# Kernel optimization log

Measured on AMD Instinct MI355X. Metric: run time of the kernel, lower is better.

## Reference

```python
import jax, jax.numpy as jnp
import numpy as np

EMBED_DIM = 200
INPUT_DIM = 512


def setup_inputs() -> dict:
    key = jax.random.key(0)
    k1, k2, k3, k4 = jax.random.split(key, 4)
    B, L, T = 64, 256, 64
    x = jax.random.normal(k1, (B, L, INPUT_DIM), dtype=jnp.float32)
    y = jax.random.normal(k2, (B, T, INPUT_DIM), dtype=jnp.float32)
    # fc = nn.Linear(input_dim, embedding_dim)
    W = jax.random.normal(k3, (EMBED_DIM, INPUT_DIM), dtype=jnp.float32) * (1.0 / np.sqrt(INPUT_DIM))
    b = jax.random.normal(k4, (EMBED_DIM,), dtype=jnp.float32) * 0.01
    return {"x": x, "y": y, "W": W, "b": b}


def reference(x, y, W, b):
    # Project both modalities (last dim != embedding_dim in original triggers fc)
    xp = jnp.einsum('bld,ed->ble', x, W) + b   # B x L x E
    yp = jnp.einsum('btd,ed->bte', y, W) + b   # B x T x E
    # Pairwise matchmap: for pair (i, j), matchmap = xp[i] @ yp[j].T -> L x T
    mm = jnp.einsum('ile,jte->ijlt', xp, yp)   # B x B x L x T
    # MISA: max over L (rows of matchmap, dim 0), then mean over T
    S = jnp.max(mm, axis=2).mean(axis=2)       # B x B
    return S
```

## Files before the change

### kernel.cpp

```cpp
#include <hip/hip_runtime.h>
#include <hip/hip_bf16.h>
#include <stdint.h>

#define BB 64
#define LL 256
#define TT 64
#define DD 512
#define EE 200
#define EP 208
#define NKK 13
#define NROWS_X 16384
#define BSTRIDE 264

typedef __attribute__((ext_vector_type(8))) short short8;
typedef __attribute__((ext_vector_type(4))) float floatx4;
typedef __attribute__((ext_vector_type(16))) float floatx16;

__device__ __forceinline__ short f2bf(float f) {
  uint32_t u = __builtin_bit_cast(uint32_t, f);
  u = (u + 0x7fffu + ((u >> 16) & 1u)) >> 16;
  return (short)u;
}

__device__ __forceinline__ uint32_t pack2(float lo, float hi) {
  return __builtin_amdgcn_perm(__builtin_bit_cast(uint32_t, hi),
                               __builtin_bit_cast(uint32_t, lo), 0x07060302u);
}

typedef const __attribute__((address_space(1))) uint32_t gu32_t;
typedef __attribute__((address_space(3))) uint32_t lu32_t;
__device__ __forceinline__ void glds16(const void* g, void* l) {
  __builtin_amdgcn_global_load_lds((gu32_t*)g, (lu32_t*)l, 16, 0, 0);
}

#define VMCNT_BARRIER(N) asm volatile("s_waitcnt vmcnt(" #N ")\n\ts_barrier" ::: "memory")

__global__ void wcvt_kernel(const float* __restrict__ W, short* __restrict__ Wb) {
  const int t = blockIdx.x * 256 + threadIdx.x;
  const int base = t * 8;
  const int e = base >> 9;
  short8 o;
  if (e < EE) {
    const floatx4 f0 = *(const floatx4*)(W + base);
    const floatx4 f1 = *(const floatx4*)(W + base + 4);
    o[0] = f2bf(f0.x); o[1] = f2bf(f0.y); o[2] = f2bf(f0.z); o[3] = f2bf(f0.w);
    o[4] = f2bf(f1.x); o[5] = f2bf(f1.y); o[6] = f2bf(f1.z); o[7] = f2bf(f1.w);
  } else {
    o = (short8)0;
  }
  *(short8*)(Wb + base) = o;
}

__global__ __launch_bounds__(256, 2) void proj_kernel(const float* __restrict__ x,
                                                      const float* __restrict__ y,
                                                      const short* __restrict__ Wb,
                                                      const float* __restrict__ bias,
                                                      short* __restrict__ pT) {
  __shared__ __align__(16) char smem[73728];
  float* ldsA = (float*)smem;
  short* ldsB = (short*)(smem + 24576);
  short* bounce = (short*)smem;

  const int tid  = threadIdx.x;
  const int lane = tid & 63;
  const int wid  = tid >> 6;
  const int r16   = lane & 15;
  const int khalf = lane >> 4;

  const int row0 = blockIdx.x * 64;
  const float* srcbase = (row0 < NROWS_X) ? (x + (size_t)row0 * DD)
                                          : (y + (size_t)(row0 - NROWS_X) * DD);

  floatx4 acc[NKK];
#pragma unroll
  for (int n = 0; n < NKK; n++) acc[n] = (floatx4){0.f, 0.f, 0.f, 0.f};

  auto stage = [&](int buf, int ks) {
#pragma unroll
    for (int it = 0; it < 2; it++) {
      const int p = it * 256 + tid;
      const int r = p >> 3, c = p & 7;
      glds16(srcbase + (size_t)r * DD + ks * 32 + ((c ^ (r & 7)) << 2),
             &ldsA[buf * 2048 + p * 4]);
    }
#pragma unroll
    for (int it = 0; it < 4; it++) {
      const int p = it * 256 + tid;
      const int r = p >> 2, c = p & 3;
      const int sr = (r < EP) ? r : (EP - 1);
      glds16(Wb + (size_t)sr * DD + ks * 32 + ((c ^ ((sr >> 1) & 3)) << 3),
             &ldsB[buf * 8192 + p * 8]);
    }
  };

  auto compute = [&](int s) {
    const int buf = s % 3;
    const int r = wid * 16 + r16;
    const int c0 = (2 * khalf) ^ (r16 & 7);
    const int c1 = (2 * khalf + 1) ^ (r16 & 7);
    const floatx4 f0 = *(const floatx4*)&ldsA[buf * 2048 + r * 32 + c0 * 4];
    const floatx4 f1 = *(const floatx4*)&ldsA[buf * 2048 + r * 32 + c1 * 4];
    union { short8 s8; uint32_t u[4]; } af;
    af.u[0] = pack2(f0.x, f0.y);
    af.u[1] = pack2(f0.z, f0.w);
    af.u[2] = pack2(f1.x, f1.y);
    af.u[3] = pack2(f1.z, f1.w);
    const int bcol = (khalf ^ ((r16 >> 1) & 3)) << 3;
#pragma unroll
    for (int n = 0; n < NKK; n++) {
      const int erow = n * 16 + r16;
      const short8 bfrag = *(const short8*)&ldsB[buf * 8192 + erow * 32 + bcol];
      acc[n] = __builtin_amdgcn_mfma_f32_16x16x32_bf16(af.s8, bfrag, acc[n], 0, 0, 0);
    }
  };

  stage(0, 0);
  stage(1, 1);

  for (int s = 0; s < 15; s++) {
    VMCNT_BARRIER(6);
    if (s + 2 < 16) stage((s + 2) % 3, s + 2);
    compute(s);
  }
  VMCNT_BARRIER(0);
  compute(15);

  __syncthreads();

#pragma unroll
  for (int n = 0; n < NKK; n++) {
    const int e = n * 16 + r16;
    const float bv = (e < EE) ? bias[e] : 0.0f;
#pragma unroll
    for (int rr = 0; rr < 4; rr++) {
      const int lr = wid * 16 + khalf * 4 + rr;
      bounce[lr * BSTRIDE + e] = f2bf(acc[n][rr] + bv);
    }
  }
  __syncthreads();

  const int rowblk0 = blockIdx.x * 2;
  for (int c = tid; c < 1664; c += 256) {
    const int q  = c >> 6;
    const int mt = (q >= 13) ? 1 : 0;
    const int n  = q - mt * 13;
    const int l  = c & 63;
    const int lr = mt * 32 + (l & 31);
    const short8 piece = *(const short8*)&bounce[lr * BSTRIDE + n * 16 + (l >> 5) * 8];
    *(short8*)&pT[((size_t)((rowblk0 + mt) * 13 + n)) * 512 + l * 8] = piece;
  }
}

__global__ __launch_bounds__(512, 2) void pair_kernel(const short* __restrict__ xpT,
                                                      const short* __restrict__ ypT,
                                                      float* __restrict__ S) {
  __shared__ __align__(16) char lds[2 * 53248 + 16384];
  float* red = (float*)(lds + 2 * 53248);

  const int tid  = threadIdx.x;
  const int lane = tid & 63;
  const int wid  = tid >> 6;
  const int jj2  = wid >> 2;
  const int wj   = wid & 3;
  const int bid  = blockIdx.x;
  const int i    = bid & 63;
  const int jq   = bid >> 6;
  const int jbase = jq * 16;

  short8 a0[NKK], a1[NKK];
  {
    const short* ab0 = xpT + ((size_t)((i * 8 + wj * 2 + 0) * NKK)) * 512 + lane * 8;
    const short* ab1 = xpT + ((size_t)((i * 8 + wj * 2 + 1) * NKK)) * 512 + lane * 8;
#pragma unroll
    for (int kk = 0; kk < NKK; kk++) {
      a0[kk] = *(const short8*)(ab0 + kk * 512);
      a1[kk] = *(const short8*)(ab1 + kk * 512);
    }
  }

  auto stageB = [&](int g) {
    const short* src = ypT + (size_t)(jbase + g * 2) * 26 * 512;
    char* dst = lds + (g & 1) * 53248;
    for (int c = tid; c < 3328; c += 512)
      glds16(src + (size_t)c * 8, dst + c * 16);
  };

  stageB(0);
  __syncthreads();

  for (int g = 0; g < 8; g++) {
    if (g + 1 < 8) stageB(g + 1);

    const int j = g * 2 + jj2;
    const short* bbase = (const short*)(lds + (g & 1) * 53248) +
                         (size_t)(jj2 * 26 * 512) + lane * 8;

    floatx16 accA0n0, accA0n1, accA1n0, accA1n1;
#pragma unroll
    for (int r = 0; r < 16; r++) {
      accA0n0[r] = 0.f; accA0n1[r] = 0.f; accA1n0[r] = 0.f; accA1n1[r] = 0.f;
    }

#pragma unroll
    for (int kk = 0; kk < NKK; kk++) {
      const short8 b0 = *(const short8*)(bbase + (0 * NKK + kk) * 512);
      const short8 b1 = *(const short8*)(bbase + (1 * NKK + kk) * 512);
      accA0n0 = __builtin_amdgcn_mfma_f32_32x32x16_bf16(a0[kk], b0, accA0n0, 0, 0, 0);
      accA1n0 = __builtin_amdgcn_mfma_f32_32x32x16_bf16(a1[kk], b0, accA1n0, 0, 0, 0);
      accA0n1 = __builtin_amdgcn_mfma_f32_32x32x16_bf16(a0[kk], b1, accA0n1, 0, 0, 0);
      accA1n1 = __builtin_amdgcn_mfma_f32_32x32x16_bf16(a1[kk], b1, accA1n1, 0, 0, 0);
    }

    float v0 = accA0n0[0], v1 = accA0n1[0];
#pragma unroll
    for (int r = 0; r < 16; r++) {
      v0 = fmaxf(v0, accA0n0[r]); v0 = fmaxf(v0, accA1n0[r]);
      v1 = fmaxf(v1, accA0n1[r]); v1 = fmaxf(v1, accA1n1[r]);
    }
    v0 = fmaxf(v0, __shfl_xor(v0, 32, 64));
    v1 = fmaxf(v1, __shfl_xor(v1, 32, 64));
    if (lane < 32) {
      red[(j * 4 + wj) * 64 + 0 * 32 + lane] = v0;
      red[(j * 4 + wj) * 64 + 1 * 32 + lane] = v1;
    }

    __syncthreads();
  }

#pragma unroll
  for (int rep = 0; rep < 2; rep++) {
    const int j = wid * 2 + rep;
    const int t = lane;
    float v = red[(j * 4 + 0) * 64 + t];
    v = fmaxf(v, red[(j * 4 + 1) * 64 + t]);
    v = fmaxf(v, red[(j * 4 + 2) * 64 + t]);
    v = fmaxf(v, red[(j * 4 + 3) * 64 + t]);
    v += __shfl_xor(v, 1, 64);
    v += __shfl_xor(v, 2, 64);
    v += __shfl_xor(v, 4, 64);
    v += __shfl_xor(v, 8, 64);
    v += __shfl_xor(v, 16, 64);
    v += __shfl_xor(v, 32, 64);
    if (t == 0) S[i * BB + jbase + j] = v * (1.0f / 64.0f);
  }
}

extern "C" void kernel_launch(void* const* d_in, const int* in_sizes, int n_in,
                              void* d_out, int out_size, void* d_ws, size_t ws_size,
                              hipStream_t stream) {
  const float* x = (const float*)d_in[0];
  const float* y = (const float*)d_in[1];
  const float* W = (const float*)d_in[2];
  const float* b = (const float*)d_in[3];
  float* S = (float*)d_out;

  char* ws = (char*)d_ws;
  short* Wb = (short*)ws;
  short* pT = (short*)(ws + 262144);
  short* ypT = pT + (size_t)6656 * 512;

  wcvt_kernel<<<52, 256, 0, stream>>>(W, Wb);
  proj_kernel<<<320, 256, 0, stream>>>(x, y, Wb, b, pT);
  pair_kernel<<<256, 512, 0, stream>>>(pT, ypT, S);
}
```

Before: 49.33 us.

## Retile projection to 80-row blocks so 256 workgroups match CU count

The projection kernel now launches 256 workgroups of 320 threads (5 waves), each covering 80 rows, instead of 320 workgroups of 64 rows. The intent is to give one wave per CU and remove the tail wave that 320 blocks cause on a 256-CU part. It also stops loading padded W rows (only 208 rows are staged) and adds an lgkmcnt wait to the barrier. The output scatter is rewritten because a block can now span 32-row tiles and the x/y boundary, and the change trades 2-blocks-per-CU occupancy for a single larger block.

```diff
diff --git a/kernel.cpp b/kernel.cpp
--- a/kernel.cpp
+++ b/kernel.cpp
@@ -11,6 +11,7 @@
 #define NKK 13
 #define NROWS_X 16384
 #define BSTRIDE 264
+#define PBM 80
 
 typedef __attribute__((ext_vector_type(8))) short short8;
 typedef __attribute__((ext_vector_type(4))) float floatx4;
@@ -33,7 +34,7 @@
   __builtin_amdgcn_global_load_lds((gu32_t*)g, (lu32_t*)l, 16, 0, 0);
 }
 
-#define VMCNT_BARRIER(N) asm volatile("s_waitcnt vmcnt(" #N ")\n\ts_barrier" ::: "memory")
+#define VMCNT_BARRIER(N) asm volatile("s_waitcnt vmcnt(" #N ") lgkmcnt(0)\n\ts_barrier" ::: "memory")
 
 __global__ void wcvt_kernel(const float* __restrict__ W, short* __restrict__ Wb) {
   const int t = blockIdx.x * 256 + threadIdx.x;
@@ -51,14 +52,14 @@
   *(short8*)(Wb + base) = o;
 }
 
-__global__ __launch_bounds__(256, 2) void proj_kernel(const float* __restrict__ x,
+__global__ __launch_bounds__(320, 1) void proj_kernel(const float* __restrict__ x,
                                                       const float* __restrict__ y,
                                                       const short* __restrict__ Wb,
                                                       const float* __restrict__ bias,
                                                       short* __restrict__ pT) {
-  __shared__ __align__(16) char smem[73728];
+  __shared__ __align__(16) char smem[71680];
   float* ldsA = (float*)smem;
-  short* ldsB = (short*)(smem + 24576);
+  short* ldsB = (short*)(smem + 30720);
   short* bounce = (short*)smem;
 
   const int tid  = threadIdx.x;
@@ -67,9 +68,7 @@
   const int r16   = lane & 15;
   const int khalf = lane >> 4;
 
-  const int row0 = blockIdx.x * 64;
-  const float* srcbase = (row0 < NROWS_X) ? (x + (size_t)row0 * DD)
-                                          : (y + (size_t)(row0 - NROWS_X) * DD);
+  const int row0 = blockIdx.x * PBM;
 
   floatx4 acc[NKK];
 #pragma unroll
@@ -78,28 +77,32 @@
   auto stage = [&](int buf, int ks) {
 #pragma unroll
     for (int it = 0; it < 2; it++) {
-      const int p = it * 256 + tid;
+      const int p = it * 320 + tid;
       const int r = p >> 3, c = p & 7;
-      glds16(srcbase + (size_t)r * DD + ks * 32 + ((c ^ (r & 7)) << 2),
-             &ldsA[buf * 2048 + p * 4]);
-    }
-#pragma unroll
-    for (int it = 0; it < 4; it++) {
-      const int p = it * 256 + tid;
-      const int r = p >> 2, c = p & 3;
-      const int sr = (r < EP) ? r : (EP - 1);
-      glds16(Wb + (size_t)sr * DD + ks * 32 + ((c ^ ((sr >> 1) & 3)) << 3),
-             &ldsB[buf * 8192 + p * 8]);
+      const int gr = row0 + r;
+      const float* src = (gr < NROWS_X) ? (x + (size_t)gr * DD)
+                                        : (y + (size_t)(gr - NROWS_X) * DD);
+      glds16(src + ks * 32 + ((c ^ (r & 7)) << 2),
+             &ldsA[buf * 2560 + p * 4]);
+    }
+#pragma unroll
+    for (int it = 0; it < 3; it++) {
+      const int p = it * 320 + tid;
+      if (it < 2 || tid < 192) {
+        const int r = p >> 2, c = p & 3;
+        glds16(Wb + (size_t)r * DD + ks * 32 + ((c ^ ((r >> 1) & 3)) << 3),
+               &ldsB[buf * 6656 + p * 8]);
+      }
     }
   };
 
   auto compute = [&](int s) {
     const int buf = s % 3;
     const int r = wid * 16 + r16;
-    const int c0 = (2 * khalf) ^ (r16 & 7);
-    const int c1 = (2 * khalf + 1) ^ (r16 & 7);
-    const floatx4 f0 = *(const floatx4*)&ldsA[buf * 2048 + r * 32 + c0 * 4];
-    const floatx4 f1 = *(const floatx4*)&ldsA[buf * 2048 + r * 32 + c1 * 4];
+    const int c0 = (2 * khalf) ^ (r & 7);
+    const int c1 = (2 * khalf + 1) ^ (r & 7);
+    const floatx4 f0 = *(const floatx4*)&ldsA[buf * 2560 + r * 32 + c0 * 4];
+    const floatx4 f1 = *(const floatx4*)&ldsA[buf * 2560 + r * 32 + c1 * 4];
     union { short8 s8; uint32_t u[4]; } af;
     af.u[0] = pack2(f0.x, f0.y);
     af.u[1] = pack2(f0.z, f0.w);
@@ -109,7 +112,7 @@
 #pragma unroll
     for (int n = 0; n < NKK; n++) {
       const int erow = n * 16 + r16;
-      const short8 bfrag = *(const short8*)&ldsB[buf * 8192 + erow * 32 + bcol];
+      const short8 bfrag = *(const short8*)&ldsB[buf * 6656 + erow * 32 + bcol];
       acc[n] = __builtin_amdgcn_mfma_f32_16x16x32_bf16(af.s8, bfrag, acc[n], 0, 0, 0);
     }
   };
@@ -118,7 +121,7 @@
   stage(1, 1);
 
   for (int s = 0; s < 15; s++) {
-    VMCNT_BARRIER(6);
+    VMCNT_BARRIER(4);
     if (s + 2 < 16) stage((s + 2) % 3, s + 2);
     compute(s);
   }
@@ -139,15 +142,14 @@
   }
   __syncthreads();
 
-  const int rowblk0 = blockIdx.x * 2;
-  for (int c = tid; c < 1664; c += 256) {
-    const int q  = c >> 6;
-    const int mt = (q >= 13) ? 1 : 0;
-    const int n  = q - mt * 13;
-    const int l  = c & 63;
-    const int lr = mt * 32 + (l & 31);
-    const short8 piece = *(const short8*)&bounce[lr * BSTRIDE + n * 16 + (l >> 5) * 8];
-    *(short8*)&pT[((size_t)((rowblk0 + mt) * 13 + n)) * 512 + l * 8] = piece;
+  for (int c = tid; c < 2080; c += 320) {
+    const int n    = c / 160;
+    const int rem  = c - n * 160;
+    const int lrow = rem >> 1;
+    const int eh   = rem & 1;
+    const int gr   = row0 + lrow;
+    const short8 piece = *(const short8*)&bounce[lrow * BSTRIDE + n * 16 + eh * 8];
+    *(short8*)&pT[((size_t)((gr >> 5) * 13 + n)) * 512 + (size_t)(((eh << 5) | (gr & 31)) * 8)] = piece;
   }
 }
 
@@ -260,6 +262,6 @@
   short* ypT = pT + (size_t)6656 * 512;
 
   wcvt_kernel<<<52, 256, 0, stream>>>(W, Wb);
-  proj_kernel<<<320, 256, 0, stream>>>(x, y, Wb, b, pT);
+  proj_kernel<<<256, 320, 0, stream>>>(x, y, Wb, b, pT);
   pair_kernel<<<256, 512, 0, stream>>>(pT, ypT, S);
 }
```

Measured after the change: 45.43 us. 1.09x faster.
